# Kernel tuning notes

Measured on AMD Instinct MI355X. Metric: run time of the kernel, lower is better.

## Reference

```python
import jax, jax.numpy as jnp
import numpy as np

N = 8192        # num_nodes
H = 128         # h_dim
E = 131072      # num edges (avg degree 16)
NREL = 90       # num relations
NB = 8          # num_bases (block-diagonal decomposition)
SI = H // NB    # block size 16


def setup_inputs() -> dict:
    key = jax.random.key(0)
    ks = jax.random.split(key, 24)
    sc = 0.01
    n = lambda k, shape, s=sc: jax.random.normal(k, shape, dtype=jnp.float32) * s
    return {
        'node_ids': jnp.arange(N, dtype=jnp.int32),
        'src': jax.random.randint(ks[0], (E,), 0, N, dtype=jnp.int32),
        'dst': jax.random.randint(ks[1], (E,), 0, N, dtype=jnp.int32),
        'etypes': jax.random.randint(ks[2], (E,), 0, NREL, dtype=jnp.int32),
        'norm': jax.random.uniform(ks[3], (E, 1), dtype=jnp.float32),
        'eps': jax.random.normal(ks[4], (N, H), dtype=jnp.float32),
        # input embedding layer
        'embedding': n(ks[5], (N, H)),
        # RelGraphConv layer 0 ('bdd'): per-relation block-diag weights, self-loop, bias
        'W0': n(ks[6], (NREL, NB, SI, SI)),
        'loop0': n(ks[7], (H, H)),
        'b0': jnp.zeros((H,), jnp.float32),
        # RelGraphConv layer 1
        'W1': n(ks[8], (NREL, NB, SI, SI)),
        'loop1': n(ks[9], (H, H)),
        'b1': jnp.zeros((H,), jnp.float32),
        # z_layer: Linear(H, 2H)  (weights stored as (in, out))
        'Wz': n(ks[10], (H, 2 * H)),
        'bz': jnp.zeros((2 * H,), jnp.float32),
        # inter_layer (UpdateLayer): Linear(H, H) + h_bias
        'Wi': n(ks[11], (H, H)),
        'bi': jnp.zeros((H,), jnp.float32),
        'hbi': jnp.zeros((H,), jnp.float32),
        # output_layer (second UpdateLayer)
        'Wo': n(ks[12], (H, H)),
        'bo': jnp.zeros((H,), jnp.float32),
        'hbo': jnp.zeros((H,), jnp.float32),
    }


def _rgcn_bdd(h, W, loop_w, bias, src, dst, etypes, norm, act):
    # gather src features, split into NB blocks of size SI
    x = h[src].reshape(-1, NB, SI)                       # [E, NB, SI]
    Wg = W[etypes]                                       # [E, NB, SI, SI] per-edge relation block weights
    msg = jnp.einsum('ebi,ebio->ebo', x, Wg).reshape(-1, H) * norm  # [E, H]
    agg = jax.ops.segment_sum(msg, dst, num_segments=N)  # scatter-add to dst
    out = agg + bias + h @ loop_w                        # self-loop + bias
    return act(out) if act is not None else out


def reference(node_ids, src, dst, etypes, norm, eps, embedding,
              W0, loop0, b0, W1, loop1, b1,
              Wz, bz, Wi, bi, hbi, Wo, bo, hbo):
    # input layer: embedding lookup; saved as input_embed
    x0 = embedding[node_ids]                             # [N, H]
    h = _rgcn_bdd(x0, W0, loop0, b0, src, dst, etypes, norm, jax.nn.relu)
    h = _rgcn_bdd(h, W1, loop1, b1, src, dst, etypes, norm, None)
    # VAE head: z ~ N(mean, exp(log_std))
    zml = h @ Wz + bz                                    # [N, 2H]
    z_mean, z_log_std = jnp.split(zml, 2, axis=-1)
    z = z_mean + jnp.exp(z_log_std) * eps                # reparameterized sample
    # decode 1: outer-product reconstruction + fused update
    R = z @ z.T                                          # [N, N]
    h = R @ (z @ Wi + bi) + R @ x0 + hbi
    # decode 2
    R2 = h @ h.T                                         # [N, N]
    out = R2 @ (h @ Wo + bo) + R2 @ x0 + hbo
    return out
```

## Files before the change

kernel.cpp:

```cpp
#include <hip/hip_runtime.h>
#include <hip/hip_bf16.h>
#include <math.h>

#define Hdim 128
#define NBq 8
#define SIq 16
#define LDP 136
#define SKX 64

typedef __attribute__((ext_vector_type(8))) short short8x;
typedef __attribute__((ext_vector_type(8))) _Float16 half8x;
typedef __attribute__((ext_vector_type(4))) float f32x4;
typedef __attribute__((ext_vector_type(4))) unsigned short ushort4x;
typedef __attribute__((ext_vector_type(2))) _Float16 half2x;

__device__ inline unsigned short f2b(float f) {
  unsigned int u = __float_as_uint(f);
  return (unsigned short)((u + 0x7fffu + ((u >> 16) & 1u)) >> 16);
}
__device__ inline unsigned int pack2(float lo, float hi) {
  return (unsigned int)f2b(lo) | ((unsigned int)f2b(hi) << 16);
}
__device__ inline unsigned short f2h(float f) {
  _Float16 h = (_Float16)f;
// ... 3 lines not shown
}
__device__ inline float h2f(unsigned short u) {
  _Float16 h;
  __builtin_memcpy(&h, &u, 2);
  return (float)h;
}
__device__ inline half2x u2h(unsigned int u) {
  union { unsigned int u; half2x h; } v;
  v.u = u;
  return v.h;
}
__device__ inline float b2f(unsigned short u) {
  return __uint_as_float(((unsigned int)u) << 16);
}

__global__ __launch_bounds__(256) void k_pre(
    const float* __restrict__ emb, const int* __restrict__ ids, float* __restrict__ x0,
    unsigned short* __restrict__ x0h,
    const float* __restrict__ W0, unsigned short* __restrict__ Wt0,
    const float* __restrict__ W1, unsigned short* __restrict__ Wt1, int w0elems,
    const float* __restrict__ l0, const float* __restrict__ l1,
    const float* __restrict__ Wi, const float* __restrict__ Wo, const float* __restrict__ Wz,
    unsigned short* __restrict__ l0t, unsigned short* __restrict__ l1t,
    unsigned short* __restrict__ Wit, unsigned short* __restrict__ Wot,
    unsigned short* __restrict__ Wzt,
    const int* __restrict__ dst, int* __restrict__ cnt, int E,
    int b1, int b2, int b3) {
  int bx = blockIdx.x, t = threadIdx.x;
  if (bx < b1) {
    int idx = bx * 256 + t;
    int n = idx >> 5, c4 = idx & 31;
    int s = ids[n];
    float4 v = ((const float4*)emb)[(size_t)s * 32 + c4];
    ((float4*)x0)[(size_t)n * 32 + c4] = v;
    ushort4x h;
    h.x = f2h(v.x); h.y = f2h(v.y); h.z = f2h(v.z); h.w = f2h(v.w);
    ((ushort4x*)x0h)[(size_t)n * 32 + c4] = h;
  } else if (bx < b2) {
    int idx = (bx - b1) * 256 + t;
    const float* W = (idx < w0elems) ? W0 : W1;
    unsigned short* Wt = (idx < w0elems) ? Wt0 : Wt1;
    int local = (idx < w0elems) ? idx : idx - w0elems;
    int rb = local >> 8, io = local & 255;
    int i = io >> 4, o = io & 15;
    Wt[(size_t)rb * 256 + o * 16 + i] = f2h(W[(size_t)rb * 256 + i * 16 + o]);
  } else if (bx < b3) {
    int idx = (bx - b2) * 256 + t;
    if (idx < 65536) {
      int w = idx >> 14, local = idx & 16383;
      const float* in = (w == 0) ? l0 : (w == 1) ? l1 : (w == 2) ? Wi : Wo;
      unsigned short* out = (w == 0) ? l0t : (w == 1) ? l1t : (w == 2) ? Wit : Wot;
      int n = local >> 7, k = local & 127;
      out[local] = f2b(in[k * 128 + n]);
    } else {
      int local = idx - 65536;
      int n = local >> 7, k = local & 127;
      Wzt[local] = f2b(Wz[k * 256 + n]);
    }
  } else {
    int e = (bx - b3) * 256 + t;
    if (e < E) atomicAdd(&cnt[dst[e]], 1);
  }
}

__global__ __launch_bounds__(1024) void k_scan(const int* __restrict__ cnt,
                                               int* __restrict__ off,
                                               int* __restrict__ cur, int N, int E) {
  __shared__ int part[1024];
  int t = threadIdx.x;
  int ipt = N / 1024;
  int base = t * ipt;
  int loc[8];
  int s = 0;
  for (int i = 0; i < ipt; ++i) { loc[i] = s; s += cnt[base + i]; }
  part[t] = s;
  __syncthreads();
  for (int d = 1; d < 1024; d <<= 1) {
    int v = part[t];
    int add = (t >= d) ? part[t - d] : 0;
    __syncthreads();
    part[t] = v + add;
    __syncthreads();
  }
  int pre = (t == 0) ? 0 : part[t - 1];
  for (int i = 0; i < ipt; ++i) {
    int o = pre + loc[i];
    off[base + i] = o;
    cur[base + i] = o;
  }
  if (t == 0) off[N] = E;
}

__global__ void k_scatter(const int* __restrict__ src, const int* __restrict__ dst,
                          const int* __restrict__ et, const float* __restrict__ norm,
                          int* __restrict__ cur, int4* __restrict__ pedge, int E) {
  int e = blockIdx.x * blockDim.x + threadIdx.x;
  if (e >= E) return;
  int p = atomicAdd(&cur[dst[e]], 1);
  pedge[p] = make_int4(src[e], et[e], __float_as_int(norm[e]), 0);
}

__global__ __launch_bounds__(128) void k_edge(
    const unsigned short* __restrict__ xh, const unsigned short* __restrict__ Wt,
    const int* __restrict__ off, const int4* __restrict__ pedge,
    float* __restrict__ agg) {
  int n = blockIdx.x;
  int f = threadIdx.x;
  int b = f >> 4, o = f & 15;
  int j0 = off[n], j1 = off[n + 1];
  float acc = 0.f;
#pragma unroll 2
  for (int j = j0; j < j1; ++j) {
    int4 meta = pedge[j];
    int s = meta.x;
    int r = meta.y;
    float nv = __int_as_float(meta.z);
    const uint4* xp = (const uint4*)(xh + (size_t)s * Hdim + b * SIq);
    const uint4* wp = (const uint4*)(Wt + ((size_t)r * NBq + b) * 256 + o * SIq);
    uint4 xa = xp[0], xc = xp[1];
    uint4 wa = wp[0], wc = wp[1];
#if __has_builtin(__builtin_amdgcn_fdot2)
    float d0 = 0.f, d1 = 0.f;
    d0 = __builtin_amdgcn_fdot2(u2h(xa.x), u2h(wa.x), d0, false);
    d1 = __builtin_amdgcn_fdot2(u2h(xa.y), u2h(wa.y), d1, false);
    d0 = __builtin_amdgcn_fdot2(u2h(xa.z), u2h(wa.z), d0, false);
    d1 = __builtin_amdgcn_fdot2(u2h(xa.w), u2h(wa.w), d1, false);
    d0 = __builtin_amdgcn_fdot2(u2h(xc.x), u2h(wc.x), d0, false);
    d1 = __builtin_amdgcn_fdot2(u2h(xc.y), u2h(wc.y), d1, false);
    d0 = __builtin_amdgcn_fdot2(u2h(xc.z), u2h(wc.z), d0, false);
    d1 = __builtin_amdgcn_fdot2(u2h(xc.w), u2h(wc.w), d1, false);
    acc = fmaf(d0 + d1, nv, acc);
#else
    float d = 0.f;
    unsigned int xu[8] = {xa.x, xa.y, xa.z, xa.w, xc.x, xc.y, xc.z, xc.w};
    unsigned int wu[8] = {wa.x, wa.y, wa.z, wa.w, wc.x, wc.y, wc.z, wc.w};
#pragma unroll
    for (int k = 0; k < 8; ++k) {
      half2x xv = u2h(xu[k]), wv = u2h(wu[k]);
      d += (float)xv.x * (float)wv.x + (float)xv.y * (float)wv.y;
    }
    acc = fmaf(d, nv, acc);
#endif
  }
  agg[(size_t)n * Hdim + f] = acc;
}

__global__ __launch_bounds__(256) void k_bgemm(
    const float* __restrict__ A, const unsigned short* __restrict__ Bt,
    float* __restrict__ C,
    const float* __restrict__ addm, const float* __restrict__ bias,
    int M, int Nc, int relu, unsigned short* __restrict__ Ch) {
  __shared__ unsigned short Al[32][136];
  __shared__ unsigned short Bl[64][136];
  int t = threadIdx.x;
  int bm = blockIdx.x * 32, bn = blockIdx.y * 64;
  {
    int r = t >> 3, c0 = (t & 7) << 4;
    const float4* ap = (const float4*)(A + (size_t)(bm + r) * Hdim + c0);
    float4 a0 = ap[0], a1 = ap[1], a2 = ap[2], a3 = ap[3];
    uint4 p0 = { pack2(a0.x, a0.y), pack2(a0.z, a0.w), pack2(a1.x, a1.y), pack2(a1.z, a1.w) };
    uint4 p1 = { pack2(a2.x, a2.y), pack2(a2.z, a2.w), pack2(a3.x, a3.y), pack2(a3.z, a3.w) };
    *(uint4*)&Al[r][c0]     = p0;
    *(uint4*)&Al[r][c0 + 8] = p1;
  }
  {
    int n = t >> 2, k0 = (t & 3) << 5;
    const uint4* bp = (const uint4*)(Bt + (size_t)(bn + n) * Hdim + k0);
    uint4 b0 = bp[0], b1 = bp[1], b2 = bp[2], b3 = bp[3];
    *(uint4*)&Bl[n][k0]      = b0;
    *(uint4*)&Bl[n][k0 + 8]  = b1;
    *(uint4*)&Bl[n][k0 + 16] = b2;
    *(uint4*)&Bl[n][k0 + 24] = b3;
  }
  __syncthreads();
  int wv = t >> 6, ln = t & 63;
  int mt = wv & 1;
  int nt0 = (wv >> 1) << 1;
  int lm = ln & 15, lk = ln >> 4;
  f32x4 acc0 = {0.f, 0.f, 0.f, 0.f}, acc1 = {0.f, 0.f, 0.f, 0.f};
#pragma unroll
  for (int ks = 0; ks < 4; ++ks) {
    short8x af = *(const short8x*)&Al[mt * 16 + lm][ks * 32 + lk * 8];
    short8x bf0 = *(const short8x*)&Bl[nt0 * 16 + lm][ks * 32 + lk * 8];
    short8x bf1 = *(const short8x*)&Bl[(nt0 + 1) * 16 + lm][ks * 32 + lk * 8];
    acc0 = __builtin_amdgcn_mfma_f32_16x16x32_bf16(af, bf0, acc0, 0, 0, 0);
    acc1 = __builtin_amdgcn_mfma_f32_16x16x32_bf16(af, bf1, acc1, 0, 0, 0);
  }
  int gcol0 = bn + nt0 * 16 + lm;
  int gcol1 = gcol0 + 16;
  float b0v = bias ? bias[gcol0] : 0.f;
  float b1v = bias ? bias[gcol1] : 0.f;
#pragma unroll
  for (int reg = 0; reg < 4; ++reg) {
    int grow = bm + mt * 16 + lk * 4 + reg;
    size_t o0 = (size_t)grow * Nc + gcol0;
    size_t o1 = (size_t)grow * Nc + gcol1;
    float v0 = acc0[reg] + b0v;
    float v1 = acc1[reg] + b1v;
    if (addm) { v0 += addm[o0]; v1 += addm[o1]; }
    if (relu) { v0 = fmaxf(v0, 0.f); v1 = fmaxf(v1, 0.f); }
    C[o0] = v0;
    C[o1] = v1;
    if (Ch) { Ch[o0] = f2h(v0); Ch[o1] = f2h(v1); }
  }
}

__global__ __launch_bounds__(256) void k_bgemm_z(
    const float* __restrict__ A, const unsigned short* __restrict__ Wzt,
    const float* __restrict__ bz, const float* __restrict__ eps,
    float* __restrict__ Z, int M, float* __restrict__ gz) {
  __shared__ unsigned short Al[32][136];
  __shared__ unsigned short Bm[64][136];
  __shared__ unsigned short Bl[64][136];
  int t = threadIdx.x;
  int bm = blockIdx.x * 32, bn = blockIdx.y * 64;
  if (gz && blockIdx.x == 0 && blockIdx.y == 0 && t < 64)
    ((float4*)gz)[t] = make_float4(0.f, 0.f, 0.f, 0.f);
  {
    int r = t >> 3, c0 = (t & 7) << 4;
    const float4* ap = (const float4*)(A + (size_t)(bm + r) * Hdim + c0);
    float4 a0 = ap[0], a1 = ap[1], a2 = ap[2], a3 = ap[3];
    uint4 p0 = { pack2(a0.x, a0.y), pack2(a0.z, a0.w), pack2(a1.x, a1.y), pack2(a1.z, a1.w) };
    uint4 p1 = { pack2(a2.x, a2.y), pack2(a2.z, a2.w), pack2(a3.x, a3.y), pack2(a3.z, a3.w) };
    *(uint4*)&Al[r][c0]     = p0;
    *(uint4*)&Al[r][c0 + 8] = p1;
  }
  {
    int n = t >> 2, k0 = (t & 3) << 5;
    const uint4* mp = (const uint4*)(Wzt + (size_t)(bn + n) * Hdim + k0);
    const uint4* lp = (const uint4*)(Wzt + (size_t)(bn + 128 + n) * Hdim + k0);
    uint4 m0 = mp[0], m1 = mp[1], m2 = mp[2], m3 = mp[3];
    uint4 l0 = lp[0], l1 = lp[1], l2 = lp[2], l3 = lp[3];
    *(uint4*)&Bm[n][k0]      = m0; *(uint4*)&Bm[n][k0 + 8]  = m1;
    *(uint4*)&Bm[n][k0 + 16] = m2; *(uint4*)&Bm[n][k0 + 24] = m3;
    *(uint4*)&Bl[n][k0]      = l0; *(uint4*)&Bl[n][k0 + 8]  = l1;
    *(uint4*)&Bl[n][k0 + 16] = l2; *(uint4*)&Bl[n][k0 + 24] = l3;
  }
  __syncthreads();
  int wv = t >> 6, ln = t & 63;
  int mt = wv & 1;
  int nt0 = (wv >> 1) << 1;
  int lm = ln & 15, lk = ln >> 4;
  f32x4 am0 = {0,0,0,0}, am1 = {0,0,0,0}, al0 = {0,0,0,0}, al1 = {0,0,0,0};
#pragma unroll
  for (int ks = 0; ks < 4; ++ks) {
    short8x af = *(const short8x*)&Al[mt * 16 + lm][ks * 32 + lk * 8];
    short8x bm0 = *(const short8x*)&Bm[nt0 * 16 + lm][ks * 32 + lk * 8];
    short8x bm1 = *(const short8x*)&Bm[(nt0 + 1) * 16 + lm][ks * 32 + lk * 8];
    short8x bl0 = *(const short8x*)&Bl[nt0 * 16 + lm][ks * 32 + lk * 8];
    short8x bl1 = *(const short8x*)&Bl[(nt0 + 1) * 16 + lm][ks * 32 + lk * 8];
    am0 = __builtin_amdgcn_mfma_f32_16x16x32_bf16(af, bm0, am0, 0, 0, 0);
    am1 = __builtin_amdgcn_mfma_f32_16x16x32_bf16(af, bm1, am1, 0, 0, 0);
    al0 = __builtin_amdgcn_mfma_f32_16x16x32_bf16(af, bl0, al0, 0, 0, 0);
    al1 = __builtin_amdgcn_mfma_f32_16x16x32_bf16(af, bl1, al1, 0, 0, 0);
  }
  int gcol0 = bn + nt0 * 16 + lm;
  int gcol1 = gcol0 + 16;
  float bm0v = bz[gcol0], bm1v = bz[gcol1];
  float bl0v = bz[128 + gcol0], bl1v = bz[128 + gcol1];
#pragma unroll
  for (int reg = 0; reg < 4; ++reg) {
    int grow = bm + mt * 16 + lk * 4 + reg;
    size_t o0 = (size_t)grow * Hdim + gcol0;
    size_t o1 = (size_t)grow * Hdim + gcol1;
    Z[o0] = am0[reg] + bm0v + expf(al0[reg] + bl0v) * eps[o0];
    Z[o1] = am1[reg] + bm1v + expf(al1[reg] + bl1v) * eps[o1];
  }
}

__global__ __launch_bounds__(256) void k_xty2m(
    const float* __restrict__ Z, const unsigned short* __restrict__ X0h,
    float* __restrict__ part, float* __restrict__ s1, float* __restrict__ cx0, int N) {
  int kc = blockIdx.x, yt = blockIdx.y;
  int t = threadIdx.x;
  int KC = N / SKX;
  int k0 = kc * KC;
  if (yt == 4) {
    int c = t & 127;
    float acc = 0.f;
    if (t >> 7) {
      for (int i = 0; i < KC; ++i)
        acc += h2f(X0h[(size_t)(k0 + i) * Hdim + c]);
      atomicAdd(cx0 + c, acc);
    } else {
      for (int i = 0; i < KC; ++i)
        acc += Z[(size_t)(k0 + i) * Hdim + c];
      atomicAdd(s1 + c, acc);
    }
    return;
  }
  __shared__ unsigned short Asl[128][72];
  __shared__ unsigned short Bsl[64][72];
  int wv = t >> 6, ln = t & 63, lm = ln & 15, lk = ln >> 4;
  int sn = t & 63, sq = t >> 6;
  f32x4 acc[8];
#pragma unroll
  for (int i = 0; i < 8; ++i) acc[i] = (f32x4){0.f, 0.f, 0.f, 0.f};
  for (int ch = 0; ch < KC; ch += 64) {
    int nrow = k0 + ch + sn;
    unsigned short atmp[32];
    {
      const float4* zr = (const float4*)(Z + (size_t)nrow * Hdim + sq * 32);
#pragma unroll
      for (int u = 0; u < 8; ++u) {
        float4 v = zr[u];
        atmp[u * 4 + 0] = f2h(v.x);
        atmp[u * 4 + 1] = f2h(v.y);
        atmp[u * 4 + 2] = f2h(v.z);
        atmp[u * 4 + 3] = f2h(v.w);
      }
    }
    unsigned short btmp[16];
    if (yt < 2) {
      const float4* zr = (const float4*)(Z + (size_t)nrow * Hdim + yt * 64 + sq * 16);
#pragma unroll
      for (int u = 0; u < 4; ++u) {
        float4 v = zr[u];
        btmp[u * 4 + 0] = f2h(v.x);
        btmp[u * 4 + 1] = f2h(v.y);
        btmp[u * 4 + 2] = f2h(v.z);
        btmp[u * 4 + 3] = f2h(v.w);
      }
    } else {
      const uint4* xr = (const uint4*)(X0h + (size_t)nrow * Hdim + (yt - 2) * 64 + sq * 16);
#pragma unroll
      for (int u = 0; u < 2; ++u) {
        uint4 v = xr[u];
        __builtin_memcpy(&btmp[u * 8], &v, 16);
      }
    }
    __syncthreads();
#pragma unroll
    for (int q = 0; q < 32; ++q) Asl[sq * 32 + q][sn] = atmp[q];
#pragma unroll
    for (int q = 0; q < 16; ++q) Bsl[sq * 16 + q][sn] = btmp[q];
    __syncthreads();
#pragma unroll
    for (int ks = 0; ks < 2; ++ks) {
      half8x bf = *(const half8x*)&Bsl[wv * 16 + lm][ks * 32 + lk * 8];
#pragma unroll
      for (int mi = 0; mi < 8; ++mi) {
        half8x af = *(const half8x*)&Asl[mi * 16 + lm][ks * 32 + lk * 8];
        acc[mi] = __builtin_amdgcn_mfma_f32_16x16x32_f16(af, bf, acc[mi], 0, 0, 0);
      }
    }
  }
  int gcol = yt * 64 + wv * 16 + lm;
  float* pb = part + (size_t)kc * (128 * 256) + gcol;
#pragma unroll
  for (int mi = 0; mi < 8; ++mi)
#pragma unroll
    for (int rg = 0; rg < 4; ++rg)
      pb[(size_t)(mi * 16 + lk * 4 + rg) * 256] = acc[mi][rg];
}

__global__ __launch_bounds__(256) void k_red(const float* __restrict__ part,
                                             float* __restrict__ SP) {
  int idx = blockIdx.x * 256 + threadIdx.x;
  float a = 0.f;
#pragma unroll 8
  for (int s = 0; s < SKX; ++s) a += part[(size_t)s * 32768 + idx];
  SP[idx] = a;
}

__device__ inline void stage_f32(unsigned short* dst, const float* __restrict__ src,
                                 int ldF, int t) {
#pragma unroll
  for (int it = 0; it < 2; ++it) {
    int id = it * 1024 + t; int row = id >> 4, ch = id & 15;
    const float4* gp = (const float4*)(src + (size_t)row * ldF) + ch * 2;
    float4 u = gp[0], v = gp[1];
    uint4 pk = { pack2(u.x, u.y), pack2(u.z, u.w), pack2(v.x, v.y), pack2(v.z, v.w) };
    *(uint4*)&dst[row * LDP + ch * 8] = pk;
  }
}
__device__ inline void stage_b16(unsigned short* dst, const unsigned short* __restrict__ src,
                                 int t) {
// ... 216 lines not shown
  const float* bo       = (const float*)d_in[19];
  const float* hbo      = (const float*)d_in[20];
  float* out = (float*)d_out;

  const int N  = in_sizes[0];
  const int E  = in_sizes[1];
  const int RB = in_sizes[7] / (SIq * SIq);

  char* ws = (char*)d_ws;
  const size_t MB = 1u << 20;
  const size_t KB = 1u << 10;
  float* X0   = (float*)(ws + 0 * MB);
  float* B1p  = (float*)(ws + 4 * MB);
  float* B2p  = (float*)(ws + 8 * MB);
  float* AGG  = (float*)(ws + 12 * MB);
  float* part = (float*)(ws + 8 * MB);
  float* SPb  = (float*)(ws + 16 * MB);
  float* s1p  = SPb + 32768;
  float* cx0p = SPb + 32896;
  unsigned short* G12t = (unsigned short*)(ws + 16 * MB + 576 * KB);
  float* bvec = (float*)(ws + 16 * MB + 640 * KB);
  int*   offp = (int*)(ws + 17 * MB);
  int*   curp = (int*)(ws + 17 * MB + 128 * KB);
  int*   cntp = (int*)(ws + 17 * MB + 256 * KB);
  int4*  pedge = (int4*)(ws + 18 * MB);
  unsigned short* Wt0 = (unsigned short*)(ws + 20 * MB);
  unsigned short* Wt1 = (unsigned short*)(ws + 20 * MB + 512 * KB);
  unsigned short* l0t = (unsigned short*)(ws + 21 * MB);
  unsigned short* l1t = (unsigned short*)(ws + 21 * MB + 64 * KB);
  unsigned short* Wit = (unsigned short*)(ws + 21 * MB + 128 * KB);
  unsigned short* Wot = (unsigned short*)(ws + 21 * MB + 192 * KB);
  unsigned short* Wzt = (unsigned short*)(ws + 21 * MB + 256 * KB);
  unsigned short* X0H = (unsigned short*)(ws + 22 * MB);
  unsigned short* B1H = (unsigned short*)(ws + 24 * MB);

  dim3 blk(256);

  const int w0elems = RB * 256;
  const int gB   = (N * 32) / 256;
  const int wtbB = (2 * w0elems + 255) / 256;
  const int wttB = 98304 / 256;
  const int histB = (E + 255) / 256;
  const int b1s = gB, b2s = gB + wtbB, b3s = gB + wtbB + wttB;
  hipMemsetAsync(cntp, 0, (size_t)N * sizeof(int), stream);
  k_pre<<<dim3(b3s + histB), blk, 0, stream>>>(
      emb, node_ids, X0, X0H, W0, Wt0, W1, Wt1, w0elems,
      loop0, loop1, Wi, Wo, Wz, l0t, l1t, Wit, Wot, Wzt,
      dst, cntp, E, b1s, b2s, b3s);
  k_scan<<<dim3(1), dim3(1024), 0, stream>>>(cntp, offp, curp, N, E);
  k_scatter<<<dim3((E + 255) / 256), blk, 0, stream>>>(src, dst, et, norm, curp, pedge, E);

  k_edge<<<dim3(N), dim3(128), 0, stream>>>(X0H, Wt0, offp, pedge, AGG);
  k_bgemm<<<dim3(N / 32, 2), blk, 0, stream>>>(X0, l0t, B1p, AGG, b0, N, Hdim, 1, B1H);
  k_edge<<<dim3(N), dim3(128), 0, stream>>>(B1H, Wt1, offp, pedge, AGG);
  k_bgemm<<<dim3(N / 32, 2), blk, 0, stream>>>(B1p, l1t, B2p, AGG, b1, N, Hdim, 0, nullptr);
  k_bgemm_z<<<dim3(N / 32, 2), blk, 0, stream>>>(B2p, Wzt, bz, eps, B1p, N, s1p);
  k_xty2m<<<dim3(SKX, 5), blk, 0, stream>>>(B1p, X0H, part, s1p, cx0p, N);
  k_red<<<dim3(128), blk, 0, stream>>>(part, SPb);
  k_fix<<<dim3(1), dim3(1024), 0, stream>>>(SPb, s1p, cx0p, Wit, Wot, bi, hbi, bo, hbo,
                                            G12t, bvec, (float)N);
  k_bgemm<<<dim3(N / 32, 2), blk, 0, stream>>>(B1p, G12t, out, nullptr, bvec, N, Hdim, 0, nullptr);
}
```

Measured before the change: 261.1 us.

## Fuse preprocessing, RGCN layers, VAE head and Gram reduction into one cooperative kernel

Replaces the chain of separate launches (preprocess, scan, scatter, two edge passes, three GEMMs, the split-K Gram product and its reduction) with one persistent cooperative kernel that separates the phases with grid-wide syncs. The split-K partial buffer and its reduction kernel are dropped; partial Gram products are now accumulated straight into the result with atomics. The goal is to remove launch overhead and the extra memory traffic of the partial buffer. In exchange, each phase runs on a fixed grid sized by occupancy and loops over its work, grid syncs add their own cost, and float atomics make the summation order nondeterministic.

```diff
diff --git a/kernel.cpp b/kernel.cpp
--- a/kernel.cpp
+++ b/kernel.cpp
@@ -1,12 +1,15 @@
 #include <hip/hip_runtime.h>
+#include <hip/hip_cooperative_groups.h>
 #include <hip/hip_bf16.h>
 #include <math.h>
+
+namespace cg = cooperative_groups;
 
 #define Hdim 128
 #define NBq 8
 #define SIq 16
 #define LDP 136
-#define SKX 64
+#define SMEGA 28672
 
 typedef __attribute__((ext_vector_type(8))) short short8x;
 typedef __attribute__((ext_vector_type(8))) _Float16 half8x;
@@ -41,353 +44,388 @@
   return __uint_as_float(((unsigned int)u) << 16);
 }
 
-__global__ __launch_bounds__(256) void k_pre(
-    const float* __restrict__ emb, const int* __restrict__ ids, float* __restrict__ x0,
-    unsigned short* __restrict__ x0h,
-    const float* __restrict__ W0, unsigned short* __restrict__ Wt0,
-    const float* __restrict__ W1, unsigned short* __restrict__ Wt1, int w0elems,
+
+__device__ __forceinline__ void edge_phase(
+    const unsigned short* __restrict__ xh, const unsigned short* __restrict__ Wt,
+    const int* __restrict__ off, const int4* __restrict__ pedge,
+    float* __restrict__ agg, int N, int bid, int nb, int t) {
+  int half = t >> 7, f = t & 127;
+  int b = f >> 4, o = f & 15;
+  for (int pr = bid; pr < (N >> 1); pr += nb) {
+    int n = pr * 2 + half;
+    int j0 = off[n], j1 = off[n + 1];
+    float acc = 0.f;
+#pragma unroll 2
+    for (int j = j0; j < j1; ++j) {
+      int4 meta = pedge[j];
+      int s = meta.x;
+      int r = meta.y;
+      float nv = __int_as_float(meta.z);
+      const uint4* xp = (const uint4*)(xh + (size_t)s * Hdim + b * SIq);
+      const uint4* wp = (const uint4*)(Wt + ((size_t)r * NBq + b) * 256 + o * SIq);
+      uint4 xa = xp[0], xc = xp[1];
+      uint4 wa = wp[0], wc = wp[1];
+#if __has_builtin(__builtin_amdgcn_fdot2)
+      float d0 = 0.f, d1 = 0.f;
+      d0 = __builtin_amdgcn_fdot2(u2h(xa.x), u2h(wa.x), d0, false);
+      d1 = __builtin_amdgcn_fdot2(u2h(xa.y), u2h(wa.y), d1, false);
+      d0 = __builtin_amdgcn_fdot2(u2h(xa.z), u2h(wa.z), d0, false);
+      d1 = __builtin_amdgcn_fdot2(u2h(xa.w), u2h(wa.w), d1, false);
+      d0 = __builtin_amdgcn_fdot2(u2h(xc.x), u2h(wc.x), d0, false);
+      d1 = __builtin_amdgcn_fdot2(u2h(xc.y), u2h(wc.y), d1, false);
+      d0 = __builtin_amdgcn_fdot2(u2h(xc.z), u2h(wc.z), d0, false);
+      d1 = __builtin_amdgcn_fdot2(u2h(xc.w), u2h(wc.w), d1, false);
+      acc = fmaf(d0 + d1, nv, acc);
+#else
+      float d = 0.f;
+      unsigned int xu[8] = {xa.x, xa.y, xa.z, xa.w, xc.x, xc.y, xc.z, xc.w};
+      unsigned int wu[8] = {wa.x, wa.y, wa.z, wa.w, wc.x, wc.y, wc.z, wc.w};
+#pragma unroll
+      for (int k = 0; k < 8; ++k) {
+        half2x xv = u2h(xu[k]), wv = u2h(wu[k]);
+        d += (float)xv.x * (float)wv.x + (float)xv.y * (float)wv.y;
+      }
+      acc = fmaf(d, nv, acc);
+#endif
+    }
+    agg[(size_t)n * Hdim + f] = acc;
+  }
+}
+
+__device__ __forceinline__ void bgemm_phase(
+    const float* __restrict__ A, const unsigned short* __restrict__ Bt,
+    float* __restrict__ C, const float* __restrict__ addm,
+    const float* __restrict__ bias, int M, int relu,
+    unsigned short* __restrict__ Ch, char* smem, int bid, int nb, int t) {
+  unsigned short (*Al)[136] = (unsigned short (*)[136])smem;
+  unsigned short (*Bl)[136] = (unsigned short (*)[136])(smem + 8704);
+  int ntile = (M >> 5) << 1;
+  int wv = t >> 6, ln = t & 63;
+  int mt = wv & 1;
+  int nt0 = (wv >> 1) << 1;
+  int lm = ln & 15, lk = ln >> 4;
+  for (int tid = bid; tid < ntile; tid += nb) {
+    int bm = (tid >> 1) * 32, bn = (tid & 1) * 64;
+    {
+      int r = t >> 3, c0 = (t & 7) << 4;
+      const float4* ap = (const float4*)(A + (size_t)(bm + r) * Hdim + c0);
+      float4 a0 = ap[0], a1 = ap[1], a2 = ap[2], a3 = ap[3];
+      uint4 p0 = { pack2(a0.x, a0.y), pack2(a0.z, a0.w), pack2(a1.x, a1.y), pack2(a1.z, a1.w) };
+      uint4 p1 = { pack2(a2.x, a2.y), pack2(a2.z, a2.w), pack2(a3.x, a3.y), pack2(a3.z, a3.w) };
+      *(uint4*)&Al[r][c0]     = p0;
+      *(uint4*)&Al[r][c0 + 8] = p1;
+    }
+    {
+      int n = t >> 2, k0 = (t & 3) << 5;
+      const uint4* bp = (const uint4*)(Bt + (size_t)(bn + n) * Hdim + k0);
+      uint4 b0 = bp[0], b1 = bp[1], b2 = bp[2], b3 = bp[3];
+      *(uint4*)&Bl[n][k0]      = b0;
+      *(uint4*)&Bl[n][k0 + 8]  = b1;
+      *(uint4*)&Bl[n][k0 + 16] = b2;
+      *(uint4*)&Bl[n][k0 + 24] = b3;
+    }
+    __syncthreads();
+    f32x4 acc0 = {0.f, 0.f, 0.f, 0.f}, acc1 = {0.f, 0.f, 0.f, 0.f};
+#pragma unroll
+    for (int ks = 0; ks < 4; ++ks) {
+      short8x af = *(const short8x*)&Al[mt * 16 + lm][ks * 32 + lk * 8];
+      short8x bf0 = *(const short8x*)&Bl[nt0 * 16 + lm][ks * 32 + lk * 8];
+      short8x bf1 = *(const short8x*)&Bl[(nt0 + 1) * 16 + lm][ks * 32 + lk * 8];
+      acc0 = __builtin_amdgcn_mfma_f32_16x16x32_bf16(af, bf0, acc0, 0, 0, 0);
+      acc1 = __builtin_amdgcn_mfma_f32_16x16x32_bf16(af, bf1, acc1, 0, 0, 0);
+    }
+    int gcol0 = bn + nt0 * 16 + lm;
+    int gcol1 = gcol0 + 16;
+    float b0v = bias ? bias[gcol0] : 0.f;
+    float b1v = bias ? bias[gcol1] : 0.f;
+#pragma unroll
+    for (int reg = 0; reg < 4; ++reg) {
+      int grow = bm + mt * 16 + lk * 4 + reg;
+      size_t o0 = (size_t)grow * Hdim + gcol0;
+      size_t o1 = (size_t)grow * Hdim + gcol1;
+      float v0 = acc0[reg] + b0v;
+      float v1 = acc1[reg] + b1v;
+      if (addm) { v0 += addm[o0]; v1 += addm[o1]; }
+      if (relu) { v0 = fmaxf(v0, 0.f); v1 = fmaxf(v1, 0.f); }
+      C[o0] = v0;
+      C[o1] = v1;
+      if (Ch) { Ch[o0] = f2h(v0); Ch[o1] = f2h(v1); }
+    }
+    __syncthreads();
+  }
+}
+
+__device__ __forceinline__ void bgemmz_phase(
+    const float* __restrict__ A, const unsigned short* __restrict__ Wzt,
+    const float* __restrict__ bz, const float* __restrict__ eps,
+    float* __restrict__ Z, int M, char* smem, int bid, int nb, int t) {
+  unsigned short (*Al)[136] = (unsigned short (*)[136])smem;
+  unsigned short (*Bl)[136] = (unsigned short (*)[136])(smem + 8704);
+  int ntile = (M >> 5) << 1;
+  int wv = t >> 6, ln = t & 63;
+  int mt = wv & 1;
+  int nt0 = (wv >> 1) << 1;
+  int lm = ln & 15, lk = ln >> 4;
+  for (int tid = bid; tid < ntile; tid += nb) {
+    int bm = (tid >> 1) * 32, bn = (tid & 1) * 64;
+    {
+      int r = t >> 3, c0 = (t & 7) << 4;
+      const float4* ap = (const float4*)(A + (size_t)(bm + r) * Hdim + c0);
+      float4 a0 = ap[0], a1 = ap[1], a2 = ap[2], a3 = ap[3];
+      uint4 p0 = { pack2(a0.x, a0.y), pack2(a0.z, a0.w), pack2(a1.x, a1.y), pack2(a1.z, a1.w) };
+      uint4 p1 = { pack2(a2.x, a2.y), pack2(a2.z, a2.w), pack2(a3.x, a3.y), pack2(a3.z, a3.w) };
+      *(uint4*)&Al[r][c0]     = p0;
+      *(uint4*)&Al[r][c0 + 8] = p1;
+    }
+    {
+      int n = t >> 2, k0 = (t & 3) << 5;
+      const uint4* mp = (const uint4*)(Wzt + (size_t)(bn + n) * Hdim + k0);
+      uint4 m0 = mp[0], m1 = mp[1], m2 = mp[2], m3 = mp[3];
+      *(uint4*)&Bl[n][k0]      = m0; *(uint4*)&Bl[n][k0 + 8]  = m1;
+      *(uint4*)&Bl[n][k0 + 16] = m2; *(uint4*)&Bl[n][k0 + 24] = m3;
+    }
+    __syncthreads();
+    f32x4 am0 = {0,0,0,0}, am1 = {0,0,0,0};
+#pragma unroll
+    for (int ks = 0; ks < 4; ++ks) {
+      short8x af = *(const short8x*)&Al[mt * 16 + lm][ks * 32 + lk * 8];
+      short8x bm0 = *(const short8x*)&Bl[nt0 * 16 + lm][ks * 32 + lk * 8];
+      short8x bm1 = *(const short8x*)&Bl[(nt0 + 1) * 16 + lm][ks * 32 + lk * 8];
+      am0 = __builtin_amdgcn_mfma_f32_16x16x32_bf16(af, bm0, am0, 0, 0, 0);
+      am1 = __builtin_amdgcn_mfma_f32_16x16x32_bf16(af, bm1, am1, 0, 0, 0);
+    }
+    __syncthreads();
+    {
+      int n = t >> 2, k0 = (t & 3) << 5;
+      const uint4* lp = (const uint4*)(Wzt + (size_t)(bn + 128 + n) * Hdim + k0);
+      uint4 l0 = lp[0], l1 = lp[1], l2 = lp[2], l3 = lp[3];
+      *(uint4*)&Bl[n][k0]      = l0; *(uint4*)&Bl[n][k0 + 8]  = l1;
+      *(uint4*)&Bl[n][k0 + 16] = l2; *(uint4*)&Bl[n][k0 + 24] = l3;
+    }
+    __syncthreads();
+    f32x4 al0 = {0,0,0,0}, al1 = {0,0,0,0};
+#pragma unroll
+    for (int ks = 0; ks < 4; ++ks) {
+      short8x af = *(const short8x*)&Al[mt * 16 + lm][ks * 32 + lk * 8];
+      short8x bl0 = *(const short8x*)&Bl[nt0 * 16 + lm][ks * 32 + lk * 8];
+      short8x bl1 = *(const short8x*)&Bl[(nt0 + 1) * 16 + lm][ks * 32 + lk * 8];
+      al0 = __builtin_amdgcn_mfma_f32_16x16x32_bf16(af, bl0, al0, 0, 0, 0);
+      al1 = __builtin_amdgcn_mfma_f32_16x16x32_bf16(af, bl1, al1, 0, 0, 0);
+    }
+    int gcol0 = bn + nt0 * 16 + lm;
+    int gcol1 = gcol0 + 16;
+    float bm0v = bz[gcol0], bm1v = bz[gcol1];
+    float bl0v = bz[128 + gcol0], bl1v = bz[128 + gcol1];
+#pragma unroll
+    for (int reg = 0; reg < 4; ++reg) {
+      int grow = bm + mt * 16 + lk * 4 + reg;
+      size_t o0 = (size_t)grow * Hdim + gcol0;
+      size_t o1 = (size_t)grow * Hdim + gcol1;
+      Z[o0] = am0[reg] + bm0v + expf(al0[reg] + bl0v) * eps[o0];
+      Z[o1] = am1[reg] + bm1v + expf(al1[reg] + bl1v) * eps[o1];
+    }
+    __syncthreads();
+  }
+}
+
+__device__ __forceinline__ void xty_phase(
+    const float* __restrict__ Z, const unsigned short* __restrict__ X0h,
+    float* __restrict__ SP, float* __restrict__ s1, float* __restrict__ cx0,
+    int N, char* smem, int bid, int nb, int t) {
+  unsigned short (*Asl)[72] = (unsigned short (*)[72])smem;
+  unsigned short (*Bsl)[72] = (unsigned short (*)[72])(smem + 128 * 72 * 2);
+  int KC = N >> 6;
+  int wv = t >> 6, ln = t & 63, lm = ln & 15, lk = ln >> 4;
+  int sn = t & 63, sq = t >> 6;
+  for (int tid = bid; tid < 320; tid += nb) {
+    __syncthreads();
+    int yt = tid >> 6, kc = tid & 63;
+    int k0 = kc * KC;
+    if (yt == 4) {
+      int c = t & 127;
+      float acc = 0.f;
+      if (t >> 7) {
+        for (int i = 0; i < KC; ++i) acc += h2f(X0h[(size_t)(k0 + i) * Hdim + c]);
+        atomicAdd(cx0 + c, acc);
+      } else {
+        for (int i = 0; i < KC; ++i) acc += Z[(size_t)(k0 + i) * Hdim + c];
+        atomicAdd(s1 + c, acc);
+      }
+      continue;
+    }
+    f32x4 acc[8];
+#pragma unroll
+    for (int i = 0; i < 8; ++i) acc[i] = (f32x4){0.f, 0.f, 0.f, 0.f};
+    for (int ch = 0; ch < KC; ch += 64) {
+      int nrow = k0 + ch + sn;
+      unsigned short atmp[32];
+      {
+        const float4* zr = (const float4*)(Z + (size_t)nrow * Hdim + sq * 32);
+#pragma unroll
+        for (int u = 0; u < 8; ++u) {
+          float4 v = zr[u];
+          atmp[u * 4 + 0] = f2h(v.x);
+          atmp[u * 4 + 1] = f2h(v.y);
+          atmp[u * 4 + 2] = f2h(v.z);
+          atmp[u * 4 + 3] = f2h(v.w);
+        }
+      }
+      unsigned short btmp[16];
+      if (yt < 2) {
+        const float4* zr = (const float4*)(Z + (size_t)nrow * Hdim + yt * 64 + sq * 16);
+#pragma unroll
+        for (int u = 0; u < 4; ++u) {
+          float4 v = zr[u];
+          btmp[u * 4 + 0] = f2h(v.x);
+          btmp[u * 4 + 1] = f2h(v.y);
+          btmp[u * 4 + 2] = f2h(v.z);
+          btmp[u * 4 + 3] = f2h(v.w);
+        }
+      } else {
+        const uint4* xr = (const uint4*)(X0h + (size_t)nrow * Hdim + (yt - 2) * 64 + sq * 16);
+#pragma unroll
+        for (int u = 0; u < 2; ++u) {
+          uint4 v = xr[u];
+          __builtin_memcpy(&btmp[u * 8], &v, 16);
+        }
+      }
+      __syncthreads();
+#pragma unroll
+      for (int q = 0; q < 32; ++q) Asl[sq * 32 + q][sn] = atmp[q];
+#pragma unroll
+      for (int q = 0; q < 16; ++q) Bsl[sq * 16 + q][sn] = btmp[q];
+      __syncthreads();
+#pragma unroll
+      for (int ks = 0; ks < 2; ++ks) {
+        half8x bf = *(const half8x*)&Bsl[wv * 16 + lm][ks * 32 + lk * 8];
+#pragma unroll
+        for (int mi = 0; mi < 8; ++mi) {
+          half8x af = *(const half8x*)&Asl[mi * 16 + lm][ks * 32 + lk * 8];
+          acc[mi] = __builtin_amdgcn_mfma_f32_16x16x32_f16(af, bf, acc[mi], 0, 0, 0);
+        }
+      }
+    }
+    int gcol = yt * 64 + wv * 16 + lm;
+#pragma unroll
+    for (int mi = 0; mi < 8; ++mi)
+#pragma unroll
+      for (int rg = 0; rg < 4; ++rg)
+        atomicAdd(&SP[(size_t)(mi * 16 + lk * 4 + rg) * 256 + gcol], acc[mi][rg]);
+  }
+}
+
+__global__ __launch_bounds__(256, 4) void k_mega(
+    const float* __restrict__ emb, const int* __restrict__ ids,
+    const int* __restrict__ srcp, const int* __restrict__ dstp,
+    const int* __restrict__ etp, const float* __restrict__ normp,
+    const float* __restrict__ eps,
+    const float* __restrict__ W0, const float* __restrict__ W1,
     const float* __restrict__ l0, const float* __restrict__ l1,
-    const float* __restrict__ Wi, const float* __restrict__ Wo, const float* __restrict__ Wz,
+    const float* __restrict__ Wi, const float* __restrict__ Wo,
+    const float* __restrict__ Wz,
+    const float* __restrict__ b0, const float* __restrict__ b1,
+    const float* __restrict__ bz,
+    float* __restrict__ X0, unsigned short* __restrict__ X0H,
+    unsigned short* __restrict__ Wt0, unsigned short* __restrict__ Wt1,
     unsigned short* __restrict__ l0t, unsigned short* __restrict__ l1t,
     unsigned short* __restrict__ Wit, unsigned short* __restrict__ Wot,
     unsigned short* __restrict__ Wzt,
-    const int* __restrict__ dst, int* __restrict__ cnt, int E,
-    int b1, int b2, int b3) {
-  int bx = blockIdx.x, t = threadIdx.x;
-  if (bx < b1) {
-    int idx = bx * 256 + t;
+    int* __restrict__ cnt, int* __restrict__ off, int* __restrict__ cur,
+    int4* __restrict__ pedge,
+    float* __restrict__ AGG, float* __restrict__ B1p,
+    unsigned short* __restrict__ B1H, float* __restrict__ B2p,
+    float* __restrict__ SPb,
+    int N, int E, int w0elems) {
+  cg::grid_group grid = cg::this_grid();
+  __shared__ __align__(16) char smem[SMEGA];
+  int t = threadIdx.x, bid = blockIdx.x, nb = gridDim.x;
+  int gid = bid * 256 + t, gsz = nb * 256;
+
+  for (int i = gid; i < N; i += gsz) cnt[i] = 0;
+  for (int i = gid; i < 33024; i += gsz) SPb[i] = 0.f;
+  for (int idx = gid; idx < N * 32; idx += gsz) {
     int n = idx >> 5, c4 = idx & 31;
     int s = ids[n];
     float4 v = ((const float4*)emb)[(size_t)s * 32 + c4];
-    ((float4*)x0)[(size_t)n * 32 + c4] = v;
+    ((float4*)X0)[(size_t)n * 32 + c4] = v;
     ushort4x h;
     h.x = f2h(v.x); h.y = f2h(v.y); h.z = f2h(v.z); h.w = f2h(v.w);
-    ((ushort4x*)x0h)[(size_t)n * 32 + c4] = h;
-  } else if (bx < b2) {
-    int idx = (bx - b1) * 256 + t;
+    ((ushort4x*)X0H)[(size_t)n * 32 + c4] = h;
+  }
+  for (int idx = gid; idx < 2 * w0elems; idx += gsz) {
     const float* W = (idx < w0elems) ? W0 : W1;
     unsigned short* Wt = (idx < w0elems) ? Wt0 : Wt1;
     int local = (idx < w0elems) ? idx : idx - w0elems;
     int rb = local >> 8, io = local & 255;
     int i = io >> 4, o = io & 15;
     Wt[(size_t)rb * 256 + o * 16 + i] = f2h(W[(size_t)rb * 256 + i * 16 + o]);
-  } else if (bx < b3) {
-    int idx = (bx - b2) * 256 + t;
+  }
+  for (int idx = gid; idx < 98304; idx += gsz) {
     if (idx < 65536) {
       int w = idx >> 14, local = idx & 16383;
       const float* in = (w == 0) ? l0 : (w == 1) ? l1 : (w == 2) ? Wi : Wo;
-      unsigned short* out = (w == 0) ? l0t : (w == 1) ? l1t : (w == 2) ? Wit : Wot;
+      unsigned short* outp = (w == 0) ? l0t : (w == 1) ? l1t : (w == 2) ? Wit : Wot;
       int n = local >> 7, k = local & 127;
-      out[local] = f2b(in[k * 128 + n]);
+      outp[local] = f2b(in[k * 128 + n]);
     } else {
       int local = idx - 65536;
       int n = local >> 7, k = local & 127;
       Wzt[local] = f2b(Wz[k * 256 + n]);
     }
-  } else {
-    int e = (bx - b3) * 256 + t;
-    if (e < E) atomicAdd(&cnt[dst[e]], 1);
-  }
-}
-
-__global__ __launch_bounds__(1024) void k_scan(const int* __restrict__ cnt,
-                                               int* __restrict__ off,
-                                               int* __restrict__ cur, int N, int E) {
-  __shared__ int part[1024];
-  int t = threadIdx.x;
-  int ipt = N / 1024;
-  int base = t * ipt;
-  int loc[8];
-  int s = 0;
-  for (int i = 0; i < ipt; ++i) { loc[i] = s; s += cnt[base + i]; }
-  part[t] = s;
-  __syncthreads();
-  for (int d = 1; d < 1024; d <<= 1) {
-    int v = part[t];
-    int add = (t >= d) ? part[t - d] : 0;
+  }
+  grid.sync();
+  for (int e = gid; e < E; e += gsz) atomicAdd(&cnt[dstp[e]], 1);
+  grid.sync();
+  if (bid == 0) {
+    int* part = (int*)smem;
+    int ipt = N >> 8;
+    int base = t * ipt;
+    int loc[32];
+    int s = 0;
+    for (int i = 0; i < ipt; ++i) { loc[i] = s; s += cnt[base + i]; }
+    part[t] = s;
     __syncthreads();
-    part[t] = v + add;
-    __syncthreads();
-  }
-  int pre = (t == 0) ? 0 : part[t - 1];
-  for (int i = 0; i < ipt; ++i) {
-    int o = pre + loc[i];
-    off[base + i] = o;
-    cur[base + i] = o;
-  }
-  if (t == 0) off[N] = E;
-}
-
-__global__ void k_scatter(const int* __restrict__ src, const int* __restrict__ dst,
-                          const int* __restrict__ et, const float* __restrict__ norm,
-                          int* __restrict__ cur, int4* __restrict__ pedge, int E) {
-  int e = blockIdx.x * blockDim.x + threadIdx.x;
-  if (e >= E) return;
-  int p = atomicAdd(&cur[dst[e]], 1);
-  pedge[p] = make_int4(src[e], et[e], __float_as_int(norm[e]), 0);
-}
-
-__global__ __launch_bounds__(128) void k_edge(
-    const unsigned short* __restrict__ xh, const unsigned short* __restrict__ Wt,
-    const int* __restrict__ off, const int4* __restrict__ pedge,
-    float* __restrict__ agg) {
-  int n = blockIdx.x;
-  int f = threadIdx.x;
-  int b = f >> 4, o = f & 15;
-  int j0 = off[n], j1 = off[n + 1];
-  float acc = 0.f;
-#pragma unroll 2
-  for (int j = j0; j < j1; ++j) {
-    int4 meta = pedge[j];
-    int s = meta.x;
-    int r = meta.y;
-    float nv = __int_as_float(meta.z);
-    const uint4* xp = (const uint4*)(xh + (size_t)s * Hdim + b * SIq);
-    const uint4* wp = (const uint4*)(Wt + ((size_t)r * NBq + b) * 256 + o * SIq);
-    uint4 xa = xp[0], xc = xp[1];
-    uint4 wa = wp[0], wc = wp[1];
-#if __has_builtin(__builtin_amdgcn_fdot2)
-    float d0 = 0.f, d1 = 0.f;
-    d0 = __builtin_amdgcn_fdot2(u2h(xa.x), u2h(wa.x), d0, false);
-    d1 = __builtin_amdgcn_fdot2(u2h(xa.y), u2h(wa.y), d1, false);
-    d0 = __builtin_amdgcn_fdot2(u2h(xa.z), u2h(wa.z), d0, false);
-    d1 = __builtin_amdgcn_fdot2(u2h(xa.w), u2h(wa.w), d1, false);
-    d0 = __builtin_amdgcn_fdot2(u2h(xc.x), u2h(wc.x), d0, false);
-    d1 = __builtin_amdgcn_fdot2(u2h(xc.y), u2h(wc.y), d1, false);
-    d0 = __builtin_amdgcn_fdot2(u2h(xc.z), u2h(wc.z), d0, false);
-    d1 = __builtin_amdgcn_fdot2(u2h(xc.w), u2h(wc.w), d1, false);
-    acc = fmaf(d0 + d1, nv, acc);
-#else
-    float d = 0.f;
-    unsigned int xu[8] = {xa.x, xa.y, xa.z, xa.w, xc.x, xc.y, xc.z, xc.w};
-    unsigned int wu[8] = {wa.x, wa.y, wa.z, wa.w, wc.x, wc.y, wc.z, wc.w};
-#pragma unroll
-    for (int k = 0; k < 8; ++k) {
-      half2x xv = u2h(xu[k]), wv = u2h(wu[k]);
-      d += (float)xv.x * (float)wv.x + (float)xv.y * (float)wv.y;
-    }
-    acc = fmaf(d, nv, acc);
-#endif
-  }
-  agg[(size_t)n * Hdim + f] = acc;
+    for (int d = 1; d < 256; d <<= 1) {
+      int v = part[t];
+      int add = (t >= d) ? part[t - d] : 0;
+      __syncthreads();
+      part[t] = v + add;
+      __syncthreads();
+    }
+    int pre = (t == 0) ? 0 : part[t - 1];
+    for (int i = 0; i < ipt; ++i) {
+      int o = pre + loc[i];
+      off[base + i] = o;
+      cur[base + i] = o;
+    }
+    if (t == 0) off[N] = E;
+  }
+  grid.sync();
+  for (int e = gid; e < E; e += gsz) {
+    int p = atomicAdd(&cur[dstp[e]], 1);
+    pedge[p] = make_int4(srcp[e], etp[e], __float_as_int(normp[e]), 0);
+  }
+  grid.sync();
+  edge_phase(X0H, Wt0, off, pedge, AGG, N, bid, nb, t);
+  grid.sync();
+  bgemm_phase(X0, l0t, B1p, AGG, b0, N, 1, B1H, smem, bid, nb, t);
+  grid.sync();
+  edge_phase(B1H, Wt1, off, pedge, AGG, N, bid, nb, t);
+  grid.sync();
+  bgemm_phase(B1p, l1t, B2p, AGG, b1, N, 0, nullptr, smem, bid, nb, t);
+  grid.sync();
+  bgemmz_phase(B2p, Wzt, bz, eps, B1p, N, smem, bid, nb, t);
+  grid.sync();
+  xty_phase(B1p, X0H, SPb, SPb + 32768, SPb + 32896, N, smem, bid, nb, t);
 }
 
 __global__ __launch_bounds__(256) void k_bgemm(
     const float* __restrict__ A, const unsigned short* __restrict__ Bt,
-    float* __restrict__ C,
-    const float* __restrict__ addm, const float* __restrict__ bias,
-    int M, int Nc, int relu, unsigned short* __restrict__ Ch) {
-  __shared__ unsigned short Al[32][136];
-  __shared__ unsigned short Bl[64][136];
-  int t = threadIdx.x;
-  int bm = blockIdx.x * 32, bn = blockIdx.y * 64;
-  {
-    int r = t >> 3, c0 = (t & 7) << 4;
-    const float4* ap = (const float4*)(A + (size_t)(bm + r) * Hdim + c0);
-    float4 a0 = ap[0], a1 = ap[1], a2 = ap[2], a3 = ap[3];
-    uint4 p0 = { pack2(a0.x, a0.y), pack2(a0.z, a0.w), pack2(a1.x, a1.y), pack2(a1.z, a1.w) };
-    uint4 p1 = { pack2(a2.x, a2.y), pack2(a2.z, a2.w), pack2(a3.x, a3.y), pack2(a3.z, a3.w) };
-    *(uint4*)&Al[r][c0]     = p0;
-    *(uint4*)&Al[r][c0 + 8] = p1;
-  }
-  {
-    int n = t >> 2, k0 = (t & 3) << 5;
-    const uint4* bp = (const uint4*)(Bt + (size_t)(bn + n) * Hdim + k0);
-    uint4 b0 = bp[0], b1 = bp[1], b2 = bp[2], b3 = bp[3];
-    *(uint4*)&Bl[n][k0]      = b0;
-    *(uint4*)&Bl[n][k0 + 8]  = b1;
-    *(uint4*)&Bl[n][k0 + 16] = b2;
-    *(uint4*)&Bl[n][k0 + 24] = b3;
-  }
-  __syncthreads();
-  int wv = t >> 6, ln = t & 63;
-  int mt = wv & 1;
-  int nt0 = (wv >> 1) << 1;
-  int lm = ln & 15, lk = ln >> 4;
-  f32x4 acc0 = {0.f, 0.f, 0.f, 0.f}, acc1 = {0.f, 0.f, 0.f, 0.f};
-#pragma unroll
-  for (int ks = 0; ks < 4; ++ks) {
-    short8x af = *(const short8x*)&Al[mt * 16 + lm][ks * 32 + lk * 8];
-    short8x bf0 = *(const short8x*)&Bl[nt0 * 16 + lm][ks * 32 + lk * 8];
-    short8x bf1 = *(const short8x*)&Bl[(nt0 + 1) * 16 + lm][ks * 32 + lk * 8];
-    acc0 = __builtin_amdgcn_mfma_f32_16x16x32_bf16(af, bf0, acc0, 0, 0, 0);
-    acc1 = __builtin_amdgcn_mfma_f32_16x16x32_bf16(af, bf1, acc1, 0, 0, 0);
-  }
-  int gcol0 = bn + nt0 * 16 + lm;
-  int gcol1 = gcol0 + 16;
-  float b0v = bias ? bias[gcol0] : 0.f;
-  float b1v = bias ? bias[gcol1] : 0.f;
-#pragma unroll
-  for (int reg = 0; reg < 4; ++reg) {
-    int grow = bm + mt * 16 + lk * 4 + reg;
-    size_t o0 = (size_t)grow * Nc + gcol0;
-    size_t o1 = (size_t)grow * Nc + gcol1;
-    float v0 = acc0[reg] + b0v;
-    float v1 = acc1[reg] + b1v;
-    if (addm) { v0 += addm[o0]; v1 += addm[o1]; }
-    if (relu) { v0 = fmaxf(v0, 0.f); v1 = fmaxf(v1, 0.f); }
-    C[o0] = v0;
-    C[o1] = v1;
-    if (Ch) { Ch[o0] = f2h(v0); Ch[o1] = f2h(v1); }
-  }
-}
-
-__global__ __launch_bounds__(256) void k_bgemm_z(
-    const float* __restrict__ A, const unsigned short* __restrict__ Wzt,
-    const float* __restrict__ bz, const float* __restrict__ eps,
-    float* __restrict__ Z, int M, float* __restrict__ gz) {
-  __shared__ unsigned short Al[32][136];
-  __shared__ unsigned short Bm[64][136];
-  __shared__ unsigned short Bl[64][136];
-  int t = threadIdx.x;
-  int bm = blockIdx.x * 32, bn = blockIdx.y * 64;
-  if (gz && blockIdx.x == 0 && blockIdx.y == 0 && t < 64)
-    ((float4*)gz)[t] = make_float4(0.f, 0.f, 0.f, 0.f);
-  {
-    int r = t >> 3, c0 = (t & 7) << 4;
-    const float4* ap = (const float4*)(A + (size_t)(bm + r) * Hdim + c0);
-    float4 a0 = ap[0], a1 = ap[1], a2 = ap[2], a3 = ap[3];
-    uint4 p0 = { pack2(a0.x, a0.y), pack2(a0.z, a0.w), pack2(a1.x, a1.y), pack2(a1.z, a1.w) };
-    uint4 p1 = { pack2(a2.x, a2.y), pack2(a2.z, a2.w), pack2(a3.x, a3.y), pack2(a3.z, a3.w) };
-    *(uint4*)&Al[r][c0]     = p0;
-    *(uint4*)&Al[r][c0 + 8] = p1;
-  }
-  {
-    int n = t >> 2, k0 = (t & 3) << 5;
-    const uint4* mp = (const uint4*)(Wzt + (size_t)(bn + n) * Hdim + k0);
-    const uint4* lp = (const uint4*)(Wzt + (size_t)(bn + 128 + n) * Hdim + k0);
-    uint4 m0 = mp[0], m1 = mp[1], m2 = mp[2], m3 = mp[3];
-    uint4 l0 = lp[0], l1 = lp[1], l2 = lp[2], l3 = lp[3];
-    *(uint4*)&Bm[n][k0]      = m0; *(uint4*)&Bm[n][k0 + 8]  = m1;
-    *(uint4*)&Bm[n][k0 + 16] = m2; *(uint4*)&Bm[n][k0 + 24] = m3;
-    *(uint4*)&Bl[n][k0]      = l0; *(uint4*)&Bl[n][k0 + 8]  = l1;
-    *(uint4*)&Bl[n][k0 + 16] = l2; *(uint4*)&Bl[n][k0 + 24] = l3;
-  }
-  __syncthreads();
-  int wv = t >> 6, ln = t & 63;
-  int mt = wv & 1;
-  int nt0 = (wv >> 1) << 1;
-  int lm = ln & 15, lk = ln >> 4;
-  f32x4 am0 = {0,0,0,0}, am1 = {0,0,0,0}, al0 = {0,0,0,0}, al1 = {0,0,0,0};
-#pragma unroll
-  for (int ks = 0; ks < 4; ++ks) {
-    short8x af = *(const short8x*)&Al[mt * 16 + lm][ks * 32 + lk * 8];
-    short8x bm0 = *(const short8x*)&Bm[nt0 * 16 + lm][ks * 32 + lk * 8];
-    short8x bm1 = *(const short8x*)&Bm[(nt0 + 1) * 16 + lm][ks * 32 + lk * 8];
-    short8x bl0 = *(const short8x*)&Bl[nt0 * 16 + lm][ks * 32 + lk * 8];
-    short8x bl1 = *(const short8x*)&Bl[(nt0 + 1) * 16 + lm][ks * 32 + lk * 8];
-    am0 = __builtin_amdgcn_mfma_f32_16x16x32_bf16(af, bm0, am0, 0, 0, 0);
-    am1 = __builtin_amdgcn_mfma_f32_16x16x32_bf16(af, bm1, am1, 0, 0, 0);
-    al0 = __builtin_amdgcn_mfma_f32_16x16x32_bf16(af, bl0, al0, 0, 0, 0);
-    al1 = __builtin_amdgcn_mfma_f32_16x16x32_bf16(af, bl1, al1, 0, 0, 0);
-  }
-  int gcol0 = bn + nt0 * 16 + lm;
-  int gcol1 = gcol0 + 16;
-  float bm0v = bz[gcol0], bm1v = bz[gcol1];
-  float bl0v = bz[128 + gcol0], bl1v = bz[128 + gcol1];
-#pragma unroll
-  for (int reg = 0; reg < 4; ++reg) {
-    int grow = bm + mt * 16 + lk * 4 + reg;
-    size_t o0 = (size_t)grow * Hdim + gcol0;
-    size_t o1 = (size_t)grow * Hdim + gcol1;
-    Z[o0] = am0[reg] + bm0v + expf(al0[reg] + bl0v) * eps[o0];
-    Z[o1] = am1[reg] + bm1v + expf(al1[reg] + bl1v) * eps[o1];
-  }
-}
-
-__global__ __launch_bounds__(256) void k_xty2m(
-    const float* __restrict__ Z, const unsigned short* __restrict__ X0h,
-    float* __restrict__ part, float* __restrict__ s1, float* __restrict__ cx0, int N) {
-  int kc = blockIdx.x, yt = blockIdx.y;
-  int t = threadIdx.x;
-  int KC = N / SKX;
-  int k0 = kc * KC;
-  if (yt == 4) {
-    int c = t & 127;
-    float acc = 0.f;
-    if (t >> 7) {
-      for (int i = 0; i < KC; ++i)
-        acc += h2f(X0h[(size_t)(k0 + i) * Hdim + c]);
-      atomicAdd(cx0 + c, acc);
-    } else {
-      for (int i = 0; i < KC; ++i)
-        acc += Z[(size_t)(k0 + i) * Hdim + c];
-      atomicAdd(s1 + c, acc);
-    }
-    return;
-  }
-  __shared__ unsigned short Asl[128][72];
-  __shared__ unsigned short Bsl[64][72];
-  int wv = t >> 6, ln = t & 63, lm = ln & 15, lk = ln >> 4;
-  int sn = t & 63, sq = t >> 6;
-  f32x4 acc[8];
-#pragma unroll
-  for (int i = 0; i < 8; ++i) acc[i] = (f32x4){0.f, 0.f, 0.f, 0.f};
-  for (int ch = 0; ch < KC; ch += 64) {
-    int nrow = k0 + ch + sn;
-    unsigned short atmp[32];
-    {
-      const float4* zr = (const float4*)(Z + (size_t)nrow * Hdim + sq * 32);
-#pragma unroll
-      for (int u = 0; u < 8; ++u) {
-        float4 v = zr[u];
-        atmp[u * 4 + 0] = f2h(v.x);
-        atmp[u * 4 + 1] = f2h(v.y);
-        atmp[u * 4 + 2] = f2h(v.z);
-        atmp[u * 4 + 3] = f2h(v.w);
-      }
-    }
-    unsigned short btmp[16];
-    if (yt < 2) {
-      const float4* zr = (const float4*)(Z + (size_t)nrow * Hdim + yt * 64 + sq * 16);
-#pragma unroll
-      for (int u = 0; u < 4; ++u) {
-        float4 v = zr[u];
-        btmp[u * 4 + 0] = f2h(v.x);
-        btmp[u * 4 + 1] = f2h(v.y);
-        btmp[u * 4 + 2] = f2h(v.z);
-        btmp[u * 4 + 3] = f2h(v.w);
-      }
-    } else {
-      const uint4* xr = (const uint4*)(X0h + (size_t)nrow * Hdim + (yt - 2) * 64 + sq * 16);
-#pragma unroll
-      for (int u = 0; u < 2; ++u) {
-        uint4 v = xr[u];
-        __builtin_memcpy(&btmp[u * 8], &v, 16);
-      }
-    }
-    __syncthreads();
-#pragma unroll
-    for (int q = 0; q < 32; ++q) Asl[sq * 32 + q][sn] = atmp[q];
-#pragma unroll
-    for (int q = 0; q < 16; ++q) Bsl[sq * 16 + q][sn] = btmp[q];
-    __syncthreads();
-#pragma unroll
-    for (int ks = 0; ks < 2; ++ks) {
-      half8x bf = *(const half8x*)&Bsl[wv * 16 + lm][ks * 32 + lk * 8];
-#pragma unroll
-      for (int mi = 0; mi < 8; ++mi) {
-        half8x af = *(const half8x*)&Asl[mi * 16 + lm][ks * 32 + lk * 8];
-        acc[mi] = __builtin_amdgcn_mfma_f32_16x16x32_f16(af, bf, acc[mi], 0, 0, 0);
-      }
-    }
-  }
-  int gcol = yt * 64 + wv * 16 + lm;
-  float* pb = part + (size_t)kc * (128 * 256) + gcol;
-#pragma unroll
-  for (int mi = 0; mi < 8; ++mi)
-#pragma unroll
-    for (int rg = 0; rg < 4; ++rg)
-      pb[(size_t)(mi * 16 + lk * 4 + rg) * 256] = acc[mi][rg];
-}
-
-__global__ __launch_bounds__(256) void k_red(const float* __restrict__ part,
-                                             float* __restrict__ SP) {
-  int idx = blockIdx.x * 256 + threadIdx.x;
-  float a = 0.f;
-#pragma unroll 8
-  for (int s = 0; s < SKX; ++s) a += part[(size_t)s * 32768 + idx];
-  SP[idx] = a;
+    float* __restrict__ C, const float* __restrict__ addm,
+    const float* __restrict__ bias, int M, int relu,
+    unsigned short* __restrict__ Ch) {
+  __shared__ __align__(16) char smem[26112];
+  bgemm_phase(A, Bt, C, addm, bias, M, relu, Ch, smem, blockIdx.x, gridDim.x, threadIdx.x);
 }
 
 __device__ inline void stage_f32(unsigned short* dst, const float* __restrict__ src,
@@ -634,7 +672,6 @@
   float* B1p  = (float*)(ws + 4 * MB);
   float* B2p  = (float*)(ws + 8 * MB);
   float* AGG  = (float*)(ws + 12 * MB);
-  float* part = (float*)(ws + 8 * MB);
   float* SPb  = (float*)(ws + 16 * MB);
   float* s1p  = SPb + 32768;
   float* cx0p = SPb + 32896;
@@ -654,30 +691,33 @@
   unsigned short* X0H = (unsigned short*)(ws + 22 * MB);
   unsigned short* B1H = (unsigned short*)(ws + 24 * MB);
 
-  dim3 blk(256);
-
-  const int w0elems = RB * 256;
-  const int gB   = (N * 32) / 256;
-  const int wtbB = (2 * w0elems + 255) / 256;
-  const int wttB = 98304 / 256;
-  const int histB = (E + 255) / 256;
-  const int b1s = gB, b2s = gB + wtbB, b3s = gB + wtbB + wttB;
-  hipMemsetAsync(cntp, 0, (size_t)N * sizeof(int), stream);
-  k_pre<<<dim3(b3s + histB), blk, 0, stream>>>(
-      emb, node_ids, X0, X0H, W0, Wt0, W1, Wt1, w0elems,
-      loop0, loop1, Wi, Wo, Wz, l0t, l1t, Wit, Wot, Wzt,
-      dst, cntp, E, b1s, b2s, b3s);
-  k_scan<<<dim3(1), dim3(1024), 0, stream>>>(cntp, offp, curp, N, E);
-  k_scatter<<<dim3((E + 255) / 256), blk, 0, stream>>>(src, dst, et, norm, curp, pedge, E);
-
-  k_edge<<<dim3(N), dim3(128), 0, stream>>>(X0H, Wt0, offp, pedge, AGG);
-  k_bgemm<<<dim3(N / 32, 2), blk, 0, stream>>>(X0, l0t, B1p, AGG, b0, N, Hdim, 1, B1H);
-  k_edge<<<dim3(N), dim3(128), 0, stream>>>(B1H, Wt1, offp, pedge, AGG);
-  k_bgemm<<<dim3(N / 32, 2), blk, 0, stream>>>(B1p, l1t, B2p, AGG, b1, N, Hdim, 0, nullptr);
-  k_bgemm_z<<<dim3(N / 32, 2), blk, 0, stream>>>(B2p, Wzt, bz, eps, B1p, N, s1p);
-  k_xty2m<<<dim3(SKX, 5), blk, 0, stream>>>(B1p, X0H, part, s1p, cx0p, N);
-  k_red<<<dim3(128), blk, 0, stream>>>(part, SPb);
+  int w0elems = RB * 256;
+  int Nv = N, Ev = E, w0v = w0elems;
+
+  static int nblk = 0;
+  if (nblk == 0) {
+    int maxB = 0;
+    hipError_t err = hipOccupancyMaxActiveBlocksPerMultiprocessor(&maxB, k_mega, 256, 0);
+    if (err != hipSuccess || maxB < 1) maxB = 2;
+    if (maxB > 8) maxB = 8;
+    nblk = maxB * 256;
+  }
+
+  void* args[] = {
+    (void*)&emb, (void*)&node_ids, (void*)&src, (void*)&dst, (void*)&et, (void*)&norm,
+    (void*)&eps, (void*)&W0, (void*)&W1, (void*)&loop0, (void*)&loop1,
+    (void*)&Wi, (void*)&Wo, (void*)&Wz,
+    (void*)&b0, (void*)&b1, (void*)&bz,
+    (void*)&X0, (void*)&X0H, (void*)&Wt0, (void*)&Wt1,
+    (void*)&l0t, (void*)&l1t, (void*)&Wit, (void*)&Wot, (void*)&Wzt,
+    (void*)&cntp, (void*)&offp, (void*)&curp, (void*)&pedge,
+    (void*)&AGG, (void*)&B1p, (void*)&B1H, (void*)&B2p, (void*)&SPb,
+    (void*)&Nv, (void*)&Ev, (void*)&w0v };
+
+  hipLaunchCooperativeKernel((const void*)k_mega, dim3(nblk), dim3(256), args, 0, stream);
+
   k_fix<<<dim3(1), dim3(1024), 0, stream>>>(SPb, s1p, cx0p, Wit, Wot, bi, hbi, bo, hbo,
                                             G12t, bvec, (float)N);
-  k_bgemm<<<dim3(N / 32, 2), blk, 0, stream>>>(B1p, G12t, out, nullptr, bvec, N, Hdim, 0, nullptr);
-}
+  k_bgemm<<<dim3((N / 32) * 2), dim3(256), 0, stream>>>(B1p, G12t, out, nullptr, bvec,
+                                                        N, 0, nullptr);
+}
```

Measured after the change: 862.0 us. 3.3x slower.
